# Kernel tuning notes

Measured on AMD Instinct MI355X. Metric: run time of the kernel, lower is better.

Reference implementation:

```python
import jax, jax.numpy as jnp
import numpy as np

MAX_LANES = 5
DELTA_V = 1.0
DELTA_D = 6.0


def setup_inputs() -> dict:
    key = jax.random.key(0)
    k1, k2 = jax.random.split(key)
    targets = jax.random.randint(k1, (32, 360, 640), 0, 6, dtype=jnp.int32)
    embedding_vector = jax.random.normal(k2, (32, 4, 360, 640), dtype=jnp.float32)
    return {"targets": targets, "embedding_vector": embedding_vector}


def reference(targets, embedding_vector):
    B, C, H, W = embedding_vector.shape
    L = MAX_LANES
    P = H * W
    t = targets.reshape(B, P)                      # [B,P] labels 0..L
    e = embedding_vector.reshape(B, C, P)          # [B,C,P]

    # per-(batch, lane) segment counts and means
    onehot = (t[:, None, :] == jnp.arange(1, L + 1, dtype=t.dtype)[None, :, None])  # [B,L,P]
    counts = onehot.sum(-1)                        # [B,L] int
    valid = counts > 1                             # lane used only if >1 points
    sums = jnp.einsum('blp,bcp->blc', onehot.astype(e.dtype), e)   # [B,L,C]
    means = sums / jnp.maximum(counts, 1)[..., None].astype(e.dtype)  # [B,L,C]

    # ---- variance (pull) loss: per-point distance to its lane mean ----
    means_ext = jnp.concatenate([jnp.zeros((B, 1, C), e.dtype), means], axis=1)  # [B,L+1,C]
    mean_pix = jnp.take_along_axis(means_ext, t[..., None].astype(jnp.int32), axis=1)  # [B,P,C]
    diff = e.transpose(0, 2, 1) - mean_pix         # [B,P,C]
    sq = jnp.sum(diff * diff, axis=-1)             # [B,P]
    dist = jnp.sqrt(jnp.maximum(sq, 1e-12))
    valid_ext = jnp.concatenate([jnp.zeros((B, 1), bool), valid], axis=1)  # [B,L+1]
    pix_valid = jnp.take_along_axis(valid_ext, t.astype(jnp.int32), axis=1)  # [B,P]
    hinge = jax.nn.relu(dist - DELTA_V)
    dist_sum = jnp.sum(jnp.where(pix_valid, hinge * hinge, 0.0))
    point_count = jnp.sum(jnp.where(valid, counts, 0)).astype(e.dtype)
    dist_loss = jnp.where(point_count > 0, dist_sum / jnp.maximum(point_count, 1.0), 0.0)

    # ---- distance (push) loss: pdist over valid lane means per batch ----
    d = means[:, :, None, :] - means[:, None, :, :]          # [B,L,L,C]
    psq = jnp.sum(d * d, axis=-1)                            # [B,L,L]
    pd = jnp.sqrt(jnp.maximum(psq, 1e-12))
    iu = jnp.arange(L)
    pair_mask = valid[:, :, None] & valid[:, None, :] & (iu[:, None] < iu[None, :])  # [B,L,L]
    ph = jax.nn.relu(DELTA_D - pd)
    per_batch_sum = jnp.sum(jnp.where(pair_mask, ph * ph, 0.0), axis=(1, 2))  # [B]
    npairs = pair_mask.sum((1, 2)).astype(e.dtype)           # [B]
    batch_has = npairs > 0                                   # needs >=2 valid lanes
    var_b = jnp.where(batch_has, per_batch_sum / jnp.maximum(npairs, 1.0), 0.0)
    n_batches = batch_has.sum().astype(e.dtype)
    var_loss = jnp.where(n_batches > 0, var_b.sum() / jnp.maximum(n_batches, 1.0), 0.0)

    return dist_loss + var_loss
```

## Files before the change

kernel.cpp:

```cpp
#include <hip/hip_runtime.h>
#include <math.h>

#define B 32
#define C 4
#define P (360*640)
#define L 5
#define DELTA_V 1.0f
#define DELTA_D 6.0f

#define BLKX 45
#define ITER1 5
#define NBLK3 (B*BLKX)
#define PSTRIDE 48

__device__ __forceinline__ float waveReduce(float v) {
#pragma unroll
    for (int off = 32; off; off >>= 1) v += __shfl_down(v, off, 64);
    return v;
}

__global__ __launch_bounds__(256, 4) void seg_sums_k(const int* __restrict__ tgt,
                                                     const float* __restrict__ emb,
                                                     float* __restrict__ partial,
                                                     unsigned char* __restrict__ tpk) {
    const int x = blockIdx.x, c = blockIdx.y, b = blockIdx.z;
    const int tid = threadIdx.x;

    const int4*   t4 = (const int4*)(tgt + (size_t)b * P);
    const float4* ec = (const float4*)(emb + ((size_t)b * C + c) * P);

    int4   tv[ITER1];
    float4 ev[ITER1];
#pragma unroll
    for (int it = 0; it < ITER1; ++it) {
        const int g = (x + it * BLKX) * 256 + tid;
        tv[it] = t4[g];
        ev[it] = ec[g];
    }

    if (c == 0) {
        uchar4* tp4 = (uchar4*)(tpk + (size_t)b * P);
#pragma unroll
        for (int it = 0; it < ITER1; ++it) {
            const int g = (x + it * BLKX) * 256 + tid;
            tp4[g] = make_uchar4((unsigned char)tv[it].x, (unsigned char)tv[it].y,
                                 (unsigned char)tv[it].z, (unsigned char)tv[it].w);
        }
    }

    float s[L], n[L];
#pragma unroll
    for (int l = 0; l < L; ++l) { s[l] = 0.f; n[l] = 0.f; }

    auto acc1 = [&](int tt, float e) {
#pragma unroll
        for (int l = 0; l < L; ++l) {
            float m = (tt == l + 1) ? 1.0f : 0.0f;
            n[l] += m;
            s[l] = fmaf(m, e, s[l]);
        }
    };
#pragma unroll
    for (int it = 0; it < ITER1; ++it) {
        acc1(tv[it].x, ev[it].x);
        acc1(tv[it].y, ev[it].y);
        acc1(tv[it].z, ev[it].z);
        acc1(tv[it].w, ev[it].w);
    }

    float vals[2*L];
#pragma unroll
    for (int l = 0; l < L; ++l) { vals[l] = s[l]; vals[L + l] = n[l]; }

    __shared__ float red[4][2*L];
    const int lane = tid & 63, wave = tid >> 6;
#pragma unroll
    for (int k = 0; k < 2*L; ++k) {
        float r = waveReduce(vals[k]);
        if (lane == 0) red[wave][k] = r;
    }
    __syncthreads();
    if (tid < L) {
        const float r = red[0][tid] + red[1][tid] + red[2][tid] + red[3][tid];
        partial[((size_t)b * 25 + c * L + tid) * PSTRIDE + x] = r;
    } else if (c == 0 && tid < 2*L) {
        const float r = red[0][tid] + red[1][tid] + red[2][tid] + red[3][tid];
        partial[((size_t)b * 25 + 20 + (tid - L)) * PSTRIDE + x] = r;
    }
}

__global__ __launch_bounds__(256, 4) void pull_k(const unsigned char* __restrict__ tpk,
                                                 const float* __restrict__ emb,
                                                 const float* __restrict__ partial,
                                                 float* __restrict__ meansG,
                                                 float* __restrict__ validG,
                                                 float* __restrict__ cntvG,
                                                 float* __restrict__ pullp) {
    __shared__ float  praw[25];
    __shared__ float4 lmean[L + 1];
    __shared__ float  lvalid[L + 1];
    __shared__ float  lred[4];
    const int xb = blockIdx.x, b = blockIdx.y;
    const int tid = threadIdx.x;
    const int lane = tid & 63, wave = tid >> 6;

    for (int v = wave; v < 25; v += 4) {
        float pv = (lane < BLKX) ? partial[((size_t)b * 25 + v) * PSTRIDE + lane] : 0.f;
        pv = waveReduce(pv);
        if (lane == 0) praw[v] = pv;
    }
    __syncthreads();
    if (tid < L) {
        const float cnt = praw[20 + tid];
        const bool  vld = cnt > 1.5f;
        const float inv = 1.0f / fmaxf(cnt, 1.0f);
        float4 m = make_float4(praw[tid] * inv, praw[5 + tid] * inv,
                               praw[10 + tid] * inv, praw[15 + tid] * inv);
        lmean[tid + 1]  = m;
        lvalid[tid + 1] = vld ? 1.f : 0.f;
        if (xb == 0) {
            *(float4*)(meansG + ((size_t)b * L + tid) * 4) = m;
            validG[b * L + tid] = vld ? 1.f : 0.f;
            cntvG[b * L + tid]  = vld ? cnt : 0.f;
        }
    }
    if (tid == 8) { lmean[0] = make_float4(0.f, 0.f, 0.f, 0.f); lvalid[0] = 0.f; }
    __syncthreads();

    const uchar4* tp4 = (const uchar4*)(tpk + (size_t)b * P);
    const float4* e0  = (const float4*)(emb + ((size_t)b * C + 0) * P);
    const float4* e1  = (const float4*)(emb + ((size_t)b * C + 1) * P);
    const float4* e2  = (const float4*)(emb + ((size_t)b * C + 2) * P);
    const float4* e3  = (const float4*)(emb + ((size_t)b * C + 3) * P);

    float acc = 0.f;
    auto proc1 = [&](int tt, float v0, float v1, float v2, float v3) {
        float4 m = lmean[tt];
        float d0 = v0 - m.x, d1 = v1 - m.y, d2 = v2 - m.z, d3 = v3 - m.w;
        float sq   = d0*d0 + d1*d1 + d2*d2 + d3*d3;
        float dist = sqrtf(fmaxf(sq, 1e-12f));
        float h    = fmaxf(dist - DELTA_V, 0.f);
        acc = fmaf(lvalid[tt] * h, h, acc);
    };
    auto consume = [&](uchar4 t, const float4& a0, const float4& a1,
                       const float4& a2, const float4& a3) {
        proc1(t.x, a0.x, a1.x, a2.x, a3.x);
        proc1(t.y, a0.y, a1.y, a2.y, a3.y);
        proc1(t.z, a0.z, a1.z, a2.z, a3.z);
        proc1(t.w, a0.w, a1.w, a2.w, a3.w);
    };

    {
        const int g0 = xb * 256 + tid, g1 = (xb + BLKX) * 256 + tid;
        uchar4 t0 = tp4[g0], t1 = tp4[g1];
        float4 a0 = e0[g0], a1 = e1[g0], a2 = e2[g0], a3 = e3[g0];
        float4 b0 = e0[g1], b1 = e1[g1], b2 = e2[g1], b3 = e3[g1];
        consume(t0, a0, a1, a2, a3);
        consume(t1, b0, b1, b2, b3);
    }
    {
        const int g0 = (xb + 2*BLKX) * 256 + tid, g1 = (xb + 3*BLKX) * 256 + tid;
        uchar4 t0 = tp4[g0], t1 = tp4[g1];
        float4 a0 = e0[g0], a1 = e1[g0], a2 = e2[g0], a3 = e3[g0];
        float4 b0 = e0[g1], b1 = e1[g1], b2 = e2[g1], b3 = e3[g1];
        consume(t0, a0, a1, a2, a3);
        consume(t1, b0, b1, b2, b3);
    }
    {
        const int g0 = (xb + 4*BLKX) * 256 + tid;
        uchar4 t0 = tp4[g0];
        float4 a0 = e0[g0], a1 = e1[g0], a2 = e2[g0], a3 = e3[g0];
        consume(t0, a0, a1, a2, a3);
    }

    float r = waveReduce(acc);
    if (lane == 0) lred[wave] = r;
    __syncthreads();
    if (tid == 0)
        pullp[b * BLKX + xb] = lred[0] + lred[1] + lred[2] + lred[3];
}

__global__ __launch_bounds__(256) void finish_k(const float* __restrict__ pullp,
                                                const float* __restrict__ meansG,
                                                const float* __restrict__ validG,
                                                const float* __restrict__ cntvG,
                                                float* __restrict__ out) {
    __shared__ float red[4][4];
    const int tid = threadIdx.x;
    const int lane = tid & 63, wave = tid >> 6;

    float vb = 0.f, has = 0.f;
    if (tid < B) {
        const float* mb = meansG + tid * L * 4;
        const float* vv = validG + tid * L;
        float ssum = 0.f, np = 0.f;
#pragma unroll
        for (int i = 0; i < L; ++i)
#pragma unroll
            for (int j = i + 1; j < L; ++j) {
                float ok = vv[i] * vv[j];
                float d0 = mb[i*4+0] - mb[j*4+0];
                float d1 = mb[i*4+1] - mb[j*4+1];
                float d2 = mb[i*4+2] - mb[j*4+2];
                float d3 = mb[i*4+3] - mb[j*4+3];
                float psq = d0*d0 + d1*d1 + d2*d2 + d3*d3;
                float pd  = sqrtf(fmaxf(psq, 1e-12f));
                float ph  = fmaxf(DELTA_D - pd, 0.f);
                ssum += ok * ph * ph;
                np   += ok;
            }
        if (np > 0.f) { vb = ssum / np; has = 1.f; }
    }
    float pc = (tid < B*L) ? cntvG[tid] : 0.f;
    float ps = 0.f;
    for (int i = tid; i < NBLK3; i += 256) ps += pullp[i];

    float rvb = waveReduce(vb);
    float rhs = waveReduce(has);
    float rpc = waveReduce(pc);
    float rps = waveReduce(ps);
    if (lane == 0) { red[wave][0]=rvb; red[wave][1]=rhs; red[wave][2]=rpc; red[wave][3]=rps; }
    __syncthreads();
    if (tid == 0) {
        float svb = red[0][0]+red[1][0]+red[2][0]+red[3][0];
        float shs = red[0][1]+red[1][1]+red[2][1]+red[3][1];
        float spc = red[0][2]+red[1][2]+red[2][2]+red[3][2];
        float sps = red[0][3]+red[1][3]+red[2][3]+red[3][3];
        float var = (shs > 0.f) ? svb / shs : 0.f;
        float dl  = (spc > 0.f) ? sps / fmaxf(spc, 1.f) : 0.f;
        out[0] = dl + var;
    }
}

extern "C" void kernel_launch(void* const* d_in, const int* in_sizes, int n_in,
                              void* d_out, int out_size, void* d_ws, size_t ws_size,
                              hipStream_t stream) {
    const int*   tgt = (const int*)d_in[0];
    const float* emb = (const float*)d_in[1];

    unsigned char* tpk = (unsigned char*)d_ws;
    float* fbase   = (float*)((char*)d_ws + (size_t)B * P);
    float* partial = fbase;
    float* meansG  = partial + (size_t)B * 25 * PSTRIDE;
    float* validG  = meansG + (size_t)B * L * 4;
    float* cntvG   = validG + B * L;
    float* pullp   = cntvG + B * L;

    seg_sums_k<<<dim3(BLKX, C, B), 256, 0, stream>>>(tgt, emb, partial, tpk);
    pull_k<<<dim3(BLKX, B), 256, 0, stream>>>(tpk, emb, partial,
                                              meansG, validG, cntvG, pullp);
    finish_k<<<1, 256, 0, stream>>>(pullp, meansG, validG, cntvG, (float*)d_out);
}
```

Measured before the change: 217.0 us.

## Fuse channel dimension into segment-sum kernel to read targets once

The segment-sum kernel no longer launches one block per channel. Each block now processes all four embedding channels, so the int32 targets are loaded once instead of four times and the compare masks are shared across channels. Loads are issued two chunks at a time. The grid shrinks fourfold and register pressure rises from 25 accumulators plus 8 float4 values in flight, which may lower occupancy and memory-level parallelism.

New measurement: 339.7 us. 56.6% more time.

```diff
diff --git a/kernel.cpp b/kernel.cpp
--- a/kernel.cpp
+++ b/kernel.cpp
@@ -23,69 +23,85 @@
                                                      const float* __restrict__ emb,
                                                      float* __restrict__ partial,
                                                      unsigned char* __restrict__ tpk) {
-    const int x = blockIdx.x, c = blockIdx.y, b = blockIdx.z;
+    const int x = blockIdx.x, b = blockIdx.y;
     const int tid = threadIdx.x;
 
     const int4*   t4 = (const int4*)(tgt + (size_t)b * P);
-    const float4* ec = (const float4*)(emb + ((size_t)b * C + c) * P);
-
-    int4   tv[ITER1];
-    float4 ev[ITER1];
-#pragma unroll
-    for (int it = 0; it < ITER1; ++it) {
-        const int g = (x + it * BLKX) * 256 + tid;
-        tv[it] = t4[g];
-        ev[it] = ec[g];
-    }
-
-    if (c == 0) {
-        uchar4* tp4 = (uchar4*)(tpk + (size_t)b * P);
-#pragma unroll
-        for (int it = 0; it < ITER1; ++it) {
-            const int g = (x + it * BLKX) * 256 + tid;
-            tp4[g] = make_uchar4((unsigned char)tv[it].x, (unsigned char)tv[it].y,
-                                 (unsigned char)tv[it].z, (unsigned char)tv[it].w);
-        }
-    }
-
-    float s[L], n[L];
-#pragma unroll
-    for (int l = 0; l < L; ++l) { s[l] = 0.f; n[l] = 0.f; }
-
-    auto acc1 = [&](int tt, float e) {
+    const float4* e0 = (const float4*)(emb + ((size_t)b * C + 0) * P);
+    const float4* e1 = (const float4*)(emb + ((size_t)b * C + 1) * P);
+    const float4* e2 = (const float4*)(emb + ((size_t)b * C + 2) * P);
+    const float4* e3 = (const float4*)(emb + ((size_t)b * C + 3) * P);
+    uchar4*      tp4 = (uchar4*)(tpk + (size_t)b * P);
+
+    float s0[L], s1[L], s2[L], s3[L], n[L];
+#pragma unroll
+    for (int l = 0; l < L; ++l) { s0[l]=0.f; s1[l]=0.f; s2[l]=0.f; s3[l]=0.f; n[l]=0.f; }
+
+    auto elem = [&](int tt, float v0, float v1, float v2, float v3) {
 #pragma unroll
         for (int l = 0; l < L; ++l) {
             float m = (tt == l + 1) ? 1.0f : 0.0f;
-            n[l] += m;
-            s[l] = fmaf(m, e, s[l]);
+            n[l]  += m;
+            s0[l] = fmaf(m, v0, s0[l]);
+            s1[l] = fmaf(m, v1, s1[l]);
+            s2[l] = fmaf(m, v2, s2[l]);
+            s3[l] = fmaf(m, v3, s3[l]);
         }
     };
-#pragma unroll
-    for (int it = 0; it < ITER1; ++it) {
-        acc1(tv[it].x, ev[it].x);
-        acc1(tv[it].y, ev[it].y);
-        acc1(tv[it].z, ev[it].z);
-        acc1(tv[it].w, ev[it].w);
-    }
-
-    float vals[2*L];
-#pragma unroll
-    for (int l = 0; l < L; ++l) { vals[l] = s[l]; vals[L + l] = n[l]; }
-
-    __shared__ float red[4][2*L];
+    auto consume = [&](int g, int4 t, const float4& a0, const float4& a1,
+                       const float4& a2, const float4& a3) {
+        tp4[g] = make_uchar4((unsigned char)t.x, (unsigned char)t.y,
+                             (unsigned char)t.z, (unsigned char)t.w);
+        elem(t.x, a0.x, a1.x, a2.x, a3.x);
+        elem(t.y, a0.y, a1.y, a2.y, a3.y);
+        elem(t.z, a0.z, a1.z, a2.z, a3.z);
+        elem(t.w, a0.w, a1.w, a2.w, a3.w);
+    };
+
+    {
+        const int g0 = x * 256 + tid, g1 = (x + BLKX) * 256 + tid;
+        int4 ta = t4[g0], tb = t4[g1];
+        float4 a0 = e0[g0], a1 = e1[g0], a2 = e2[g0], a3 = e3[g0];
+        float4 b0 = e0[g1], b1 = e1[g1], b2 = e2[g1], b3 = e3[g1];
+        consume(g0, ta, a0, a1, a2, a3);
+        consume(g1, tb, b0, b1, b2, b3);
+    }
+    {
+        const int g0 = (x + 2*BLKX) * 256 + tid, g1 = (x + 3*BLKX) * 256 + tid;
+        int4 ta = t4[g0], tb = t4[g1];
+        float4 a0 = e0[g0], a1 = e1[g0], a2 = e2[g0], a3 = e3[g0];
+        float4 b0 = e0[g1], b1 = e1[g1], b2 = e2[g1], b3 = e3[g1];
+        consume(g0, ta, a0, a1, a2, a3);
+        consume(g1, tb, b0, b1, b2, b3);
+    }
+    {
+        const int g0 = (x + 4*BLKX) * 256 + tid;
+        int4 ta = t4[g0];
+        float4 a0 = e0[g0], a1 = e1[g0], a2 = e2[g0], a3 = e3[g0];
+        consume(g0, ta, a0, a1, a2, a3);
+    }
+
+    float vals[25];
+#pragma unroll
+    for (int l = 0; l < L; ++l) {
+        vals[l]      = s0[l];
+        vals[5 + l]  = s1[l];
+        vals[10 + l] = s2[l];
+        vals[15 + l] = s3[l];
+        vals[20 + l] = n[l];
+    }
+
+    __shared__ float red[4][25];
     const int lane = tid & 63, wave = tid >> 6;
 #pragma unroll
-    for (int k = 0; k < 2*L; ++k) {
+    for (int k = 0; k < 25; ++k) {
         float r = waveReduce(vals[k]);
         if (lane == 0) red[wave][k] = r;
     }
     __syncthreads();
-    if (tid < L) {
+    if (tid < 25) {
         const float r = red[0][tid] + red[1][tid] + red[2][tid] + red[3][tid];
-        partial[((size_t)b * 25 + c * L + tid) * PSTRIDE + x] = r;
-    } else if (c == 0 && tid < 2*L) {
-        const float r = red[0][tid] + red[1][tid] + red[2][tid] + red[3][tid];
-        partial[((size_t)b * 25 + 20 + (tid - L)) * PSTRIDE + x] = r;
+        partial[((size_t)b * 25 + tid) * PSTRIDE + x] = r;
     }
 }
 
@@ -246,7 +262,7 @@
     float* cntvG   = validG + B * L;
     float* pullp   = cntvG + B * L;
 
-    seg_sums_k<<<dim3(BLKX, C, B), 256, 0, stream>>>(tgt, emb, partial, tpk);
+    seg_sums_k<<<dim3(BLKX, B), 256, 0, stream>>>(tgt, emb, partial, tpk);
     pull_k<<<dim3(BLKX, B), 256, 0, stream>>>(tpk, emb, partial,
                                               meansG, validG, cntvG, pullp);
     finish_k<<<1, 256, 0, stream>>>(pullp, meansG, validG, cntvG, (float*)d_out);
```

## Map channels to waves, split means into separate kernel, finer-grained blocks

Applied to the files above, without the earlier changes.

The segment-sum kernel now assigns each of the four channels to a wave within one block instead of separate grid blocks, with 225 chunks per batch and one int4 group per lane-iteration. Mean and validity computation moves into a dedicated small kernel so the pull kernel no longer re-reduces partials in every block. The pull kernel processes one vector group per thread across many more blocks. This trades an extra launch and less per-thread memory-level parallelism for more blocks and no redundant reductions.

Result: slower. 233.6 us (+7.6%).

```diff
diff --git a/kernel.cpp b/kernel.cpp
--- a/kernel.cpp
+++ b/kernel.cpp
@@ -8,10 +8,9 @@
 #define DELTA_V 1.0f
 #define DELTA_D 6.0f
 
-#define BLKX 45
-#define ITER1 5
-#define NBLK3 (B*BLKX)
-#define PSTRIDE 48
+#define CH1 225
+#define PSTR 228
+#define NBLK3 (B*CH1)
 
 __device__ __forceinline__ float waveReduce(float v) {
 #pragma unroll
@@ -19,30 +18,30 @@
     return v;
 }
 
-__global__ __launch_bounds__(256, 4) void seg_sums_k(const int* __restrict__ tgt,
+__global__ __launch_bounds__(256, 2) void seg_sums_k(const int* __restrict__ tgt,
                                                      const float* __restrict__ emb,
                                                      float* __restrict__ partial,
                                                      unsigned char* __restrict__ tpk) {
-    const int x = blockIdx.x, c = blockIdx.y, b = blockIdx.z;
-    const int tid = threadIdx.x;
+    const int x = blockIdx.x, b = blockIdx.y;
+    const int tid = threadIdx.x;
+    const int lane = tid & 63, wave = tid >> 6;
 
     const int4*   t4 = (const int4*)(tgt + (size_t)b * P);
-    const float4* ec = (const float4*)(emb + ((size_t)b * C + c) * P);
-
-    int4   tv[ITER1];
-    float4 ev[ITER1];
-#pragma unroll
-    for (int it = 0; it < ITER1; ++it) {
-        const int g = (x + it * BLKX) * 256 + tid;
+    const float4* ec = (const float4*)(emb + ((size_t)b * C + wave) * P);
+    uchar4*      tp4 = (uchar4*)(tpk + (size_t)b * P);
+
+    int4   tv[4];
+    float4 ev[4];
+#pragma unroll
+    for (int it = 0; it < 4; ++it) {
+        const int g = x * 256 + it * 64 + lane;
         tv[it] = t4[g];
         ev[it] = ec[g];
     }
-
-    if (c == 0) {
-        uchar4* tp4 = (uchar4*)(tpk + (size_t)b * P);
-#pragma unroll
-        for (int it = 0; it < ITER1; ++it) {
-            const int g = (x + it * BLKX) * 256 + tid;
+    if (wave == 0) {
+#pragma unroll
+        for (int it = 0; it < 4; ++it) {
+            const int g = x * 256 + it * 64 + lane;
             tp4[g] = make_uchar4((unsigned char)tv[it].x, (unsigned char)tv[it].y,
                                  (unsigned char)tv[it].z, (unsigned char)tv[it].w);
         }
@@ -52,62 +51,50 @@
 #pragma unroll
     for (int l = 0; l < L; ++l) { s[l] = 0.f; n[l] = 0.f; }
 
-    auto acc1 = [&](int tt, float e) {
+    auto elem = [&](int tt, float v) {
 #pragma unroll
         for (int l = 0; l < L; ++l) {
             float m = (tt == l + 1) ? 1.0f : 0.0f;
             n[l] += m;
-            s[l] = fmaf(m, e, s[l]);
+            s[l] = fmaf(m, v, s[l]);
         }
     };
 #pragma unroll
-    for (int it = 0; it < ITER1; ++it) {
-        acc1(tv[it].x, ev[it].x);
-        acc1(tv[it].y, ev[it].y);
-        acc1(tv[it].z, ev[it].z);
-        acc1(tv[it].w, ev[it].w);
-    }
-
-    float vals[2*L];
-#pragma unroll
-    for (int l = 0; l < L; ++l) { vals[l] = s[l]; vals[L + l] = n[l]; }
-
-    __shared__ float red[4][2*L];
-    const int lane = tid & 63, wave = tid >> 6;
-#pragma unroll
-    for (int k = 0; k < 2*L; ++k) {
-        float r = waveReduce(vals[k]);
+    for (int it = 0; it < 4; ++it) {
+        elem(tv[it].x, ev[it].x);
+        elem(tv[it].y, ev[it].y);
+        elem(tv[it].z, ev[it].z);
+        elem(tv[it].w, ev[it].w);
+    }
+
+    __shared__ float red[4][2 * L];
+#pragma unroll
+    for (int k = 0; k < 2 * L; ++k) {
+        float r = waveReduce(k < L ? s[k] : n[k - L]);
         if (lane == 0) red[wave][k] = r;
     }
     __syncthreads();
-    if (tid < L) {
-        const float r = red[0][tid] + red[1][tid] + red[2][tid] + red[3][tid];
-        partial[((size_t)b * 25 + c * L + tid) * PSTRIDE + x] = r;
-    } else if (c == 0 && tid < 2*L) {
-        const float r = red[0][tid] + red[1][tid] + red[2][tid] + red[3][tid];
-        partial[((size_t)b * 25 + 20 + (tid - L)) * PSTRIDE + x] = r;
-    }
-}
-
-__global__ __launch_bounds__(256, 4) void pull_k(const unsigned char* __restrict__ tpk,
-                                                 const float* __restrict__ emb,
-                                                 const float* __restrict__ partial,
-                                                 float* __restrict__ meansG,
-                                                 float* __restrict__ validG,
-                                                 float* __restrict__ cntvG,
-                                                 float* __restrict__ pullp) {
-    __shared__ float  praw[25];
-    __shared__ float4 lmean[L + 1];
-    __shared__ float  lvalid[L + 1];
-    __shared__ float  lred[4];
-    const int xb = blockIdx.x, b = blockIdx.y;
+    if (tid < 25) {
+        const float r = (tid < 20) ? red[tid / 5][tid % 5] : red[0][L + (tid - 20)];
+        partial[((size_t)b * 25 + tid) * PSTR + x] = r;
+    }
+}
+
+__global__ __launch_bounds__(256) void means_k(const float* __restrict__ partial,
+                                               float* __restrict__ meansG,
+                                               float* __restrict__ validG,
+                                               float* __restrict__ cntvG) {
+    __shared__ float praw[25];
+    const int b = blockIdx.x;
     const int tid = threadIdx.x;
     const int lane = tid & 63, wave = tid >> 6;
 
     for (int v = wave; v < 25; v += 4) {
-        float pv = (lane < BLKX) ? partial[((size_t)b * 25 + v) * PSTRIDE + lane] : 0.f;
-        pv = waveReduce(pv);
-        if (lane == 0) praw[v] = pv;
+        float sum = 0.f;
+        for (int i = lane; i < CH1; i += 64)
+            sum += partial[((size_t)b * 25 + v) * PSTR + i];
+        sum = waveReduce(sum);
+        if (lane == 0) praw[v] = sum;
     }
     __syncthreads();
     if (tid < L) {
@@ -116,15 +103,29 @@
         const float inv = 1.0f / fmaxf(cnt, 1.0f);
         float4 m = make_float4(praw[tid] * inv, praw[5 + tid] * inv,
                                praw[10 + tid] * inv, praw[15 + tid] * inv);
-        lmean[tid + 1]  = m;
-        lvalid[tid + 1] = vld ? 1.f : 0.f;
-        if (xb == 0) {
-            *(float4*)(meansG + ((size_t)b * L + tid) * 4) = m;
-            validG[b * L + tid] = vld ? 1.f : 0.f;
-            cntvG[b * L + tid]  = vld ? cnt : 0.f;
-        }
-    }
-    if (tid == 8) { lmean[0] = make_float4(0.f, 0.f, 0.f, 0.f); lvalid[0] = 0.f; }
+        *(float4*)(meansG + ((size_t)b * L + tid) * 4) = m;
+        validG[b * L + tid] = vld ? 1.f : 0.f;
+        cntvG[b * L + tid]  = vld ? cnt : 0.f;
+    }
+}
+
+__global__ __launch_bounds__(256, 4) void pull_k(const unsigned char* __restrict__ tpk,
+                                                 const float* __restrict__ emb,
+                                                 const float* __restrict__ meansG,
+                                                 const float* __restrict__ validG,
+                                                 float* __restrict__ pullp) {
+    __shared__ float4 lmean[L + 1];
+    __shared__ float  lvalid[L + 1];
+    __shared__ float  lred[4];
+    const int x = blockIdx.x, b = blockIdx.y;
+    const int tid = threadIdx.x;
+    const int lane = tid & 63, wave = tid >> 6;
+
+    if (tid < L) {
+        lmean[tid + 1]  = *(const float4*)(meansG + ((size_t)b * L + tid) * 4);
+        lvalid[tid + 1] = validG[b * L + tid];
+    }
+    if (tid == L) { lmean[0] = make_float4(0.f, 0.f, 0.f, 0.f); lvalid[0] = 0.f; }
     __syncthreads();
 
     const uchar4* tp4 = (const uchar4*)(tpk + (size_t)b * P);
@@ -132,6 +133,10 @@
     const float4* e1  = (const float4*)(emb + ((size_t)b * C + 1) * P);
     const float4* e2  = (const float4*)(emb + ((size_t)b * C + 2) * P);
     const float4* e3  = (const float4*)(emb + ((size_t)b * C + 3) * P);
+
+    const int g = x * 256 + tid;
+    uchar4 t0 = tp4[g];
+    float4 a0 = e0[g], a1 = e1[g], a2 = e2[g], a3 = e3[g];
 
     float acc = 0.f;
     auto proc1 = [&](int tt, float v0, float v1, float v2, float v3) {
@@ -142,42 +147,16 @@
         float h    = fmaxf(dist - DELTA_V, 0.f);
         acc = fmaf(lvalid[tt] * h, h, acc);
     };
-    auto consume = [&](uchar4 t, const float4& a0, const float4& a1,
-                       const float4& a2, const float4& a3) {
-        proc1(t.x, a0.x, a1.x, a2.x, a3.x);
-        proc1(t.y, a0.y, a1.y, a2.y, a3.y);
-        proc1(t.z, a0.z, a1.z, a2.z, a3.z);
-        proc1(t.w, a0.w, a1.w, a2.w, a3.w);
-    };
-
-    {
-        const int g0 = xb * 256 + tid, g1 = (xb + BLKX) * 256 + tid;
-        uchar4 t0 = tp4[g0], t1 = tp4[g1];
-        float4 a0 = e0[g0], a1 = e1[g0], a2 = e2[g0], a3 = e3[g0];
-        float4 b0 = e0[g1], b1 = e1[g1], b2 = e2[g1], b3 = e3[g1];
-        consume(t0, a0, a1, a2, a3);
-        consume(t1, b0, b1, b2, b3);
-    }
-    {
-        const int g0 = (xb + 2*BLKX) * 256 + tid, g1 = (xb + 3*BLKX) * 256 + tid;
-        uchar4 t0 = tp4[g0], t1 = tp4[g1];
-        float4 a0 = e0[g0], a1 = e1[g0], a2 = e2[g0], a3 = e3[g0];
-        float4 b0 = e0[g1], b1 = e1[g1], b2 = e2[g1], b3 = e3[g1];
-        consume(t0, a0, a1, a2, a3);
-        consume(t1, b0, b1, b2, b3);
-    }
-    {
-        const int g0 = (xb + 4*BLKX) * 256 + tid;
-        uchar4 t0 = tp4[g0];
-        float4 a0 = e0[g0], a1 = e1[g0], a2 = e2[g0], a3 = e3[g0];
-        consume(t0, a0, a1, a2, a3);
-    }
+    proc1(t0.x, a0.x, a1.x, a2.x, a3.x);
+    proc1(t0.y, a0.y, a1.y, a2.y, a3.y);
+    proc1(t0.z, a0.z, a1.z, a2.z, a3.z);
+    proc1(t0.w, a0.w, a1.w, a2.w, a3.w);
 
     float r = waveReduce(acc);
     if (lane == 0) lred[wave] = r;
     __syncthreads();
     if (tid == 0)
-        pullp[b * BLKX + xb] = lred[0] + lred[1] + lred[2] + lred[3];
+        pullp[b * CH1 + x] = lred[0] + lred[1] + lred[2] + lred[3];
 }
 
 __global__ __launch_bounds__(256) void finish_k(const float* __restrict__ pullp,
@@ -241,13 +220,13 @@
     unsigned char* tpk = (unsigned char*)d_ws;
     float* fbase   = (float*)((char*)d_ws + (size_t)B * P);
     float* partial = fbase;
-    float* meansG  = partial + (size_t)B * 25 * PSTRIDE;
+    float* meansG  = partial + (size_t)B * 25 * PSTR;
     float* validG  = meansG + (size_t)B * L * 4;
     float* cntvG   = validG + B * L;
     float* pullp   = cntvG + B * L;
 
-    seg_sums_k<<<dim3(BLKX, C, B), 256, 0, stream>>>(tgt, emb, partial, tpk);
-    pull_k<<<dim3(BLKX, B), 256, 0, stream>>>(tpk, emb, partial,
-                                              meansG, validG, cntvG, pullp);
+    seg_sums_k<<<dim3(CH1, B), 256, 0, stream>>>(tgt, emb, partial, tpk);
+    means_k<<<dim3(B), 256, 0, stream>>>(partial, meansG, validG, cntvG);
+    pull_k<<<dim3(CH1, B), 256, 0, stream>>>(tpk, emb, meansG, validG, pullp);
     finish_k<<<1, 256, 0, stream>>>(pullp, meansG, validG, cntvG, (float*)d_out);
 }
```
